# Performance work log

Measured on AMD Instinct MI355X. Metric: run time of the kernel, lower is better.

## Reference

```python
import jax, jax.numpy as jnp
import numpy as np

B, T, D, U = 2, 512, 768, 768


def setup_inputs() -> dict:
    key = jax.random.key(0)
    kx, kv, ku, kw = jax.random.split(key, 4)
    x = jax.random.normal(kx, (B, T, D), dtype=jnp.float32)
    # glorot-ish scaled params
    V_a = jax.random.normal(kv, (U,), dtype=jnp.float32) * (1.0 / np.sqrt(U))
    U_a = jax.random.normal(ku, (D, U), dtype=jnp.float32) * (1.0 / np.sqrt(D))
    b_u = jnp.zeros((U,), dtype=jnp.float32)
    W_a = jax.random.normal(kw, (D, U), dtype=jnp.float32) * (1.0 / np.sqrt(D))
    return {"x": x, "V_a": V_a, "U_a": U_a, "b_u": b_u, "W_a": W_a}


def reference(x, V_a, U_a, b_u, W_a):
    # Bahdanau additive self-attention, fully batched (replaces the per-timestep loop).
    # wx[b,i,u] = x[b,i] @ W_a  (query projection; original recomputed this per step)
    wx = jnp.einsum('bid,du->biu', x, W_a)
    # ux[b,j,u] = x[b,j] @ U_a + b_u  (the _uxpb term)
    ux = jnp.einsum('bjd,du->bju', x, U_a) + b_u
    # e[b,i,j] = V_a . tanh(wx[b,i] + ux[b,j])
    e = jnp.einsum('biju,u->bij', jnp.tanh(wx[:, :, None, :] + ux[:, None, :, :]), V_a)
    # original: exp / sum over keys == softmax over axis j (no mask path)
    at = jax.nn.softmax(e, axis=2)
    # context[b,i,d] = sum_j at[b,i,j] * x[b,j,d]
    return jnp.einsum('bij,bjd->bid', at, x)
```

## Files before the change

kernel.cpp:

```cpp
#include <hip/hip_runtime.h>
#include <hip/hip_bf16.h>

#define BB 2
#define TT 512
#define DD 768
#define UU 768
#define NR (BB*TT)
#define CC 2.8853900817779268f
#define HC 1.4426950408889634f

typedef __attribute__((ext_vector_type(8))) short short8v;
typedef __attribute__((ext_vector_type(4))) float float4v;
typedef __attribute__((ext_vector_type(4))) unsigned short ushort4v;
typedef _Float16 half4v __attribute__((ext_vector_type(4)));

static __device__ __forceinline__ float fexp2(float x) { return __builtin_amdgcn_exp2f(x); }
static __device__ __forceinline__ float frcp(float x)  { return __builtin_amdgcn_rcpf(x); }
static __device__ __forceinline__ unsigned short bf16rn(float f) {
    unsigned u = __builtin_bit_cast(unsigned, f);
    u += 0x7FFFu + ((u >> 16) & 1u);
    return (unsigned short)(u >> 16);
}
static __device__ __forceinline__ float bf16tof(unsigned short h) {
    return __builtin_bit_cast(float, ((unsigned)h) << 16);
}

__global__ __launch_bounds__(256) void prep_split(
    const float* __restrict__ x,
    const float* __restrict__ Wm,
    const float* __restrict__ Um,
    unsigned short* __restrict__ xhi, unsigned short* __restrict__ xlo,
    unsigned short* __restrict__ WThi, unsigned short* __restrict__ WTlo,
    unsigned short* __restrict__ UThi, unsigned short* __restrict__ UTlo)
{
    const int mode = blockIdx.z;
    const int t = threadIdx.x;

    if (mode == 2) {
        const int blk = blockIdx.y * 12 + blockIdx.x;
        const float4* src = (const float4*)x + (size_t)blk * 1024;
        #pragma unroll
        for (int i = 0; i < 4; ++i) {
            const int idx = i * 256 + t;
            const float4 v = src[idx];
            ushort4v h, l;
            h.x = bf16rn(v.x); l.x = bf16rn(v.x - bf16tof(h.x));
            h.y = bf16rn(v.y); l.y = bf16rn(v.y - bf16tof(h.y));
            h.z = bf16rn(v.z); l.z = bf16rn(v.z - bf16tof(h.z));
            h.w = bf16rn(v.w); l.w = bf16rn(v.w - bf16tof(h.w));
            const size_t off = (size_t)blk * 4096 + (size_t)idx * 4;
            *(ushort4v*)(xhi + off) = h;
            *(ushort4v*)(xlo + off) = l;
        }
        return;
    }
    if (blockIdx.y >= 12) return;

    const float* __restrict__ S = (mode == 0) ? Wm : Um;
    unsigned short* __restrict__ Thi = (mode == 0) ? WThi : UThi;
    unsigned short* __restrict__ Tlo = (mode == 0) ? WTlo : UTlo;

    __shared__ float tile[64][65];
    const int d0 = blockIdx.y * 64;
    const int u0 = blockIdx.x * 64;

    #pragma unroll
    for (int i = 0; i < 4; ++i) {
        const int f4 = i * 256 + t;
        const int r  = f4 >> 4;
        const int c4 = f4 & 15;
        const float4 v = *(const float4*)(S + (size_t)(d0 + r) * UU + u0 + c4 * 4);
        tile[r][c4 * 4 + 0] = v.x;
        tile[r][c4 * 4 + 1] = v.y;
        tile[r][c4 * 4 + 2] = v.z;
        tile[r][c4 * 4 + 3] = v.w;
    }
    __syncthreads();
    #pragma unroll
    for (int i = 0; i < 2; ++i) {
        const int cid = i * 256 + t;
        const int ur  = cid >> 3;
        const int kc  = cid & 7;
        short8v H, L;
        #pragma unroll
        for (int j = 0; j < 8; ++j) {
            const float f = tile[kc * 8 + j][ur];
            const unsigned short h = bf16rn(f);
            H[j] = (short)h;
            L[j] = (short)bf16rn(f - bf16tof(h));
        }
        const size_t off = (size_t)(u0 + ur) * DD + d0 + kc * 8;
        *(short8v*)(Thi + off) = H;
        *(short8v*)(Tlo + off) = L;
    }
}

__global__ __launch_bounds__(256) void gemm_mfma(
    const unsigned short* __restrict__ xhi, const unsigned short* __restrict__ xlo,
    const unsigned short* __restrict__ WThi, const unsigned short* __restrict__ WTlo,
    const unsigned short* __restrict__ UThi, const unsigned short* __restrict__ UTlo,
    const float* __restrict__ bu,
    float* __restrict__ EW4,
    _Float16* __restrict__ EUTH)
{
    const int mode = blockIdx.z;
    const unsigned short* __restrict__ Ahi = mode ? UThi : WThi;
    const unsigned short* __restrict__ Alo = mode ? UTlo : WTlo;

    __shared__ unsigned short lds[4 * 4096];

    const int tid  = threadIdx.x;
    const int lane = tid & 63;
    const int wid  = tid >> 6;
    const int wm   = wid >> 1, wn = wid & 1;
    const int u0   = blockIdx.y * 64;
    const int r0t  = blockIdx.x * 64;

    const int srow0 = tid >> 3;
    const int srow1 = srow0 + 32;
    const int sc0   = tid & 7;
    const int sw0   = (sc0 ^ (srow0 & 7)) << 3;

    short8v g0, g1, g2, g3, g4, g5, g6, g7;

#define LOADSTEP(K0) { \
    const size_t ka = (size_t)(K0) + sc0 * 8; \
    g0 = *(const short8v*)(Ahi + (size_t)(u0 + srow0) * DD + ka); \
    g1 = *(const short8v*)(Ahi + (size_t)(u0 + srow1) * DD + ka); \
    g2 = *(const short8v*)(Alo + (size_t)(u0 + srow0) * DD + ka); \
    g3 = *(const short8v*)(Alo + (size_t)(u0 + srow1) * DD + ka); \
    g4 = *(const short8v*)(xhi + (size_t)(r0t + srow0) * DD + ka); \
    g5 = *(const short8v*)(xhi + (size_t)(r0t + srow1) * DD + ka); \
    g6 = *(const short8v*)(xlo + (size_t)(r0t + srow0) * DD + ka); \
    g7 = *(const short8v*)(xlo + (size_t)(r0t + srow1) * DD + ka); }

#define WRITESTEP { \
    *(short8v*)&lds[0 * 4096 + srow0 * 64 + sw0] = g0; \
    *(short8v*)&lds[0 * 4096 + srow1 * 64 + sw0] = g1; \
    *(short8v*)&lds[1 * 4096 + srow0 * 64 + sw0] = g2; \
    *(short8v*)&lds[1 * 4096 + srow1 * 64 + sw0] = g3; \
    *(short8v*)&lds[2 * 4096 + srow0 * 64 + sw0] = g4; \
    *(short8v*)&lds[2 * 4096 + srow1 * 64 + sw0] = g5; \
    *(short8v*)&lds[3 * 4096 + srow0 * 64 + sw0] = g6; \
    *(short8v*)&lds[3 * 4096 + srow1 * 64 + sw0] = g7; }

    float4v acc[2][2] = {};

    LOADSTEP(0);
    for (int s = 0; s < 12; ++s) {
        __syncthreads();
        WRITESTEP;
        __syncthreads();
        if (s < 11) LOADSTEP((s + 1) * 64);

        short8v ah[2][2], al[2][2], bh[2][2], bl[2][2];
        #pragma unroll
        for (int f = 0; f < 2; ++f) {
            const int arow = wm * 32 + f * 16 + (lane & 15);
            const int brow = wn * 32 + f * 16 + (lane & 15);
            #pragma unroll
            for (int kk = 0; kk < 2; ++kk) {
                const int ck = kk * 4 + (lane >> 4);
                ah[f][kk] = *(const short8v*)&lds[0 * 4096 + arow * 64 + (((ck ^ (arow & 7))) << 3)];
                al[f][kk] = *(const short8v*)&lds[1 * 4096 + arow * 64 + (((ck ^ (arow & 7))) << 3)];
                bh[f][kk] = *(const short8v*)&lds[2 * 4096 + brow * 64 + (((ck ^ (brow & 7))) << 3)];
                bl[f][kk] = *(const short8v*)&lds[3 * 4096 + brow * 64 + (((ck ^ (brow & 7))) << 3)];
            }
        }
        #pragma unroll
        for (int kk = 0; kk < 2; ++kk)
            #pragma unroll
            for (int m = 0; m < 2; ++m)
                #pragma unroll
                for (int n = 0; n < 2; ++n) {
                    acc[m][n] = __builtin_amdgcn_mfma_f32_16x16x32_bf16(ah[m][kk], bh[n][kk], acc[m][n], 0, 0, 0);
                    acc[m][n] = __builtin_amdgcn_mfma_f32_16x16x32_bf16(ah[m][kk], bl[n][kk], acc[m][n], 0, 0, 0);
                    acc[m][n] = __builtin_amdgcn_mfma_f32_16x16x32_bf16(al[m][kk], bh[n][kk], acc[m][n], 0, 0, 0);
                }
    }

    #pragma unroll
    for (int m = 0; m < 2; ++m) {
        #pragma unroll
        for (int n = 0; n < 2; ++n) {
            const int ub = u0 + wm * 32 + m * 16 + ((lane >> 4) << 2);
            const int r  = r0t + wn * 32 + n * 16 + (lane & 15);
            if (mode == 0) {
                float* dst = EW4 + ((size_t)(r >> 2) * UU + ub) * 4 + (r & 3);
                #pragma unroll
                for (int reg = 0; reg < 4; ++reg)
                    dst[reg * 4] = fexp2(acc[m][n][reg] * CC);
            } else {
                const int b = r >> 9, j = r & 511;
                const float4 bv = *(const float4*)(bu + ub);
                half4v o;
                o[0] = (_Float16)fexp2((acc[m][n][0] + bv.x) * HC);
                o[1] = (_Float16)fexp2((acc[m][n][1] + bv.y) * HC);
                o[2] = (_Float16)fexp2((acc[m][n][2] + bv.z) * HC);
                o[3] = (_Float16)fexp2((acc[m][n][3] + bv.w) * HC);
                *(half4v*)(EUTH + ((size_t)(b * 192 + (ub >> 2)) * 512 + j) * 4) = o;
            }
        }
    }
#undef LOADSTEP
#undef WRITESTEP
}

__global__ __launch_bounds__(1024) void attn_fused(
    const float* __restrict__ x,
    const float* __restrict__ V_a,
    const float* __restrict__ EW4,
    const _Float16* __restrict__ EUTH,
    float* __restrict__ out)
{
    extern __shared__ float smem[];
    float4* sw4  = (float4*)smem;
    float*  vv   = smem + 3072;
    float*  xchg = smem + 4096;
    float*  red  = smem + 6144;
    float4* at4  = (float4*)(smem + 8192);
    float*  part = smem;
    float*  iv   = smem + 12352;

    const int tid  = threadIdx.x;
    const int lane = tid & 63;
    const int j    = tid & 511;
    const int uh   = tid >> 9;

    const int bid = blockIdx.x;
    const int blk = (bid & 7) * 32 + (bid >> 3);

    const int r0 = blk * 4;
    const int b  = r0 >> 9;

    if (tid < UU) {
        sw4[tid] = ((const float4*)EW4)[(size_t)blk * UU + tid];
        vv[tid]  = V_a[tid];
    }
    __syncthreads();

    const half4v* __restrict__ eqh =
        (const half4v*)EUTH + (size_t)(b * 192 + uh * 96) * 512 + j;

    float acc0 = 0.f, acc1 = 0.f, acc2 = 0.f, acc3 = 0.f;

#define PAIR(E0, E1, u0) { \
    const float4 S0 = sw4[(u0)]; \
    const float4 S1 = sw4[(u0) + 1]; \
    const float v0 = vv[(u0)], v1 = vv[(u0) + 1]; \
    { const float da = fmaf((E0), S0.x, 1.f), db = fmaf((E1), S1.x, 1.f); \
      float n = v0 * db; n = fmaf(v1, da, n); \
      acc0 = fmaf(n, frcp(da * db), acc0); } \
    { const float da = fmaf((E0), S0.y, 1.f), db = fmaf((E1), S1.y, 1.f); \
      float n = v0 * db; n = fmaf(v1, da, n); \
      acc1 = fmaf(n, frcp(da * db), acc1); } \
    { const float da = fmaf((E0), S0.z, 1.f), db = fmaf((E1), S1.z, 1.f); \
      float n = v0 * db; n = fmaf(v1, da, n); \
      acc2 = fmaf(n, frcp(da * db), acc2); } \
    { const float da = fmaf((E0), S0.w, 1.f), db = fmaf((E1), S1.w, 1.f); \
      float n = v0 * db; n = fmaf(v1, da, n); \
      acc3 = fmaf(n, frcp(da * db), acc3); } }
#define QUADH(H, UB) { \
    const float e0 = (float)(H)[0], e1 = (float)(H)[1]; \
    const float e2 = (float)(H)[2], e3 = (float)(H)[3]; \
    PAIR(e0 * e0, e1 * e1, (UB)); PAIR(e2 * e2, e3 * e3, (UB) + 2); }

    const int ubase = uh * 384 / 4;
    const int ub0 = uh * 384;

    half4v c0 = eqh[0 * 512], c1 = eqh[1 * 512], c2 = eqh[2 * 512], c3 = eqh[3 * 512];
    #pragma unroll 1
    for (int c = 0; c < 23; ++c) {
        const int q = 4 * c;
        half4v n0 = eqh[(size_t)(q + 4) * 512];
        half4v n1 = eqh[(size_t)(q + 5) * 512];
        half4v n2 = eqh[(size_t)(q + 6) * 512];
        half4v n3 = eqh[(size_t)(q + 7) * 512];
        const int ub = ub0 + 16 * c;
        QUADH(c0, ub); QUADH(c1, ub + 4); QUADH(c2, ub + 8); QUADH(c3, ub + 12);
        c0 = n0; c1 = n1; c2 = n2; c3 = n3;
    }
    QUADH(c0, ub0 + 368); QUADH(c1, ub0 + 372); QUADH(c2, ub0 + 376); QUADH(c3, ub0 + 380);
    (void)ubase;

    if (uh) *(float4*)&xchg[j * 4] = make_float4(acc0, acc1, acc2, acc3);
    __syncthreads();
    if (!uh) {
        const float4 o = *(float4*)&xchg[j * 4];
        acc0 += o.x; acc1 += o.y; acc2 += o.z; acc3 += o.w;
    }

    float m0 = acc0, m1 = acc1, m2 = acc2, m3 = acc3;
    #pragma unroll
    for (int off = 32; off; off >>= 1) {
        m0 = fminf(m0, __shfl_xor(m0, off, 64));
        m1 = fminf(m1, __shfl_xor(m1, off, 64));
        m2 = fminf(m2, __shfl_xor(m2, off, 64));
        m3 = fminf(m3, __shfl_xor(m3, off, 64));
    }
    if (tid < 512 && lane == 0) {
        const int w = tid >> 6;
        red[0 * 8 + w] = m0; red[1 * 8 + w] = m1;
        red[2 * 8 + w] = m2; red[3 * 8 + w] = m3;
    }
    __syncthreads();
    float M0 = red[0], M1 = red[8], M2 = red[16], M3 = red[24];
    #pragma unroll
    for (int k = 1; k < 8; ++k) {
        M0 = fminf(M0, red[0 * 8 + k]);
        M1 = fminf(M1, red[1 * 8 + k]);
        M2 = fminf(M2, red[2 * 8 + k]);
        M3 = fminf(M3, red[3 * 8 + k]);
    }

    const float p0 = fexp2(CC * (M0 - acc0));
    const float p1 = fexp2(CC * (M1 - acc1));
    const float p2 = fexp2(CC * (M2 - acc2));
    const float p3 = fexp2(CC * (M3 - acc3));
    float s0 = p0, s1 = p1, s2 = p2, s3 = p3;
    #pragma unroll
    for (int off = 32; off; off >>= 1) {
        s0 += __shfl_xor(s0, off, 64);
        s1 += __shfl_xor(s1, off, 64);
        s2 += __shfl_xor(s2, off, 64);
        s3 += __shfl_xor(s3, off, 64);
    }
    __syncthreads();
    if (tid < 512 && lane == 0) {
        const int w = tid >> 6;
        red[32 + 0 * 8 + w] = s0; red[32 + 1 * 8 + w] = s1;
        red[32 + 2 * 8 + w] = s2; red[32 + 3 * 8 + w] = s3;
    }
    __syncthreads();
    if (tid == 0) {
        float S0 = red[32], S1 = red[40], S2 = red[48], S3 = red[56];
        #pragma unroll
        for (int k = 1; k < 8; ++k) {
            S0 += red[32 + k]; S1 += red[40 + k];
            S2 += red[48 + k]; S3 += red[56 + k];
        }
        iv[0] = frcp(S0); iv[1] = frcp(S1); iv[2] = frcp(S2); iv[3] = frcp(S3);
    }
    if (tid < 512) at4[j] = make_float4(p0, p1, p2, p3);
    __syncthreads();

    const int w16 = tid >> 6;
    const int jw  = w16 * 32;
    const float* __restrict__ xb = x + (size_t)b * TT * DD + (size_t)jw * DD + 4 * lane;
    float4 z4 = {0.f, 0.f, 0.f, 0.f};
    float4 pc00 = z4, pc01 = z4, pc02 = z4;
    float4 pc10 = z4, pc11 = z4, pc12 = z4;
    float4 pc20 = z4, pc21 = z4, pc22 = z4;
    float4 pc30 = z4, pc31 = z4, pc32 = z4;

#define F4(dst, a, xv) { dst.x = fmaf(a, xv.x, dst.x); dst.y = fmaf(a, xv.y, dst.y); \
                         dst.z = fmaf(a, xv.z, dst.z); dst.w = fmaf(a, xv.w, dst.w); }
    #pragma unroll 2
    for (int jj = 0; jj < 32; ++jj) {
        const float4 a = at4[jw + jj];
        const float* xr = xb + (size_t)jj * DD;
        const float4 x0 = *(const float4*)(xr);
        const float4 x1 = *(const float4*)(xr + 256);
        const float4 x2 = *(const float4*)(xr + 512);
        F4(pc00, a.x, x0); F4(pc01, a.x, x1); F4(pc02, a.x, x2);
        F4(pc10, a.y, x0); F4(pc11, a.y, x1); F4(pc12, a.y, x2);
        F4(pc20, a.z, x0); F4(pc21, a.z, x1); F4(pc22, a.z, x2);
        F4(pc30, a.w, x0); F4(pc31, a.w, x1); F4(pc32, a.w, x2);
    }
    __syncthreads();

#define REDPASS(PA, PB, PCc, R) { \
    *(float4*)&part[w16 * 772 + 4 * lane]       = PA; \
    *(float4*)&part[w16 * 772 + 256 + 4 * lane] = PB; \
    *(float4*)&part[w16 * 772 + 512 + 4 * lane] = PCc; \
    __syncthreads(); \
    if (tid < 768) { \
        float ssum = 0.f; \
        _Pragma("unroll") \
        for (int w2 = 0; w2 < 16; ++w2) ssum += part[w2 * 772 + tid]; \
        out[(size_t)(r0 + (R)) * DD + tid] = ssum * iv[(R)]; \
    } \
    __syncthreads(); }

    REDPASS(pc00, pc01, pc02, 0);
    REDPASS(pc10, pc11, pc12, 1);
    REDPASS(pc20, pc21, pc22, 2);
    REDPASS(pc30, pc31, pc32, 3);
}

extern "C" void kernel_launch(void* const* d_in, const int* in_sizes, int n_in,
                              void* d_out, int out_size, void* d_ws, size_t ws_size,
                              hipStream_t stream)
{
    const float* x   = (const float*)d_in[0];
    const float* V_a = (const float*)d_in[1];
    const float* U_a = (const float*)d_in[2];
    const float* b_u = (const float*)d_in[3];
    const float* W_a = (const float*)d_in[4];
    float* out = (float*)d_out;

    float* EW4 = (float*)d_ws;
    _Float16* EUTH = (_Float16*)(EW4 + (size_t)UU * NR);
    unsigned short* xhi  = (unsigned short*)(EUTH + (size_t)BB * UU * TT);
    unsigned short* xlo  = xhi + (size_t)NR * DD;
    unsigned short* WThi = xlo + (size_t)NR * DD;
    unsigned short* WTlo = WThi + (size_t)UU * DD;
    unsigned short* UThi = WTlo + (size_t)UU * DD;
    unsigned short* UTlo = UThi + (size_t)UU * DD;

    hipLaunchKernelGGL(prep_split, dim3(12, 16, 3), dim3(256), 0, stream,
                       x, W_a, U_a, xhi, xlo, WThi, WTlo, UThi, UTlo);

    hipLaunchKernelGGL(gemm_mfma, dim3(16, 12, 2), dim3(256), 0, stream,
                       xhi, xlo, WThi, WTlo, UThi, UTlo, b_u, EW4, EUTH);

    const int ldsB = 12356 * sizeof(float);
    hipLaunchKernelGGL(attn_fused, dim3(NR / 4), dim3(1024), ldsB, stream,
                       x, V_a, EW4, EUTH, out);
}
```

Baseline: 84.75 us.

## Store key exp terms in fp32 and combine four tanh terms per reciprocal

The key-side exponentials are now written in fp32 with the full 2*log2e scale, instead of fp16 half-scale values that had to be squared on load. The attention inner loop merges four tanh terms into one reciprocal rather than two, which cuts the number of rcp instructions. Query exponentials and V_a are read straight from global memory (uniform per block, so cached) rather than staged in LDS, which drops the preload and its barrier. The cost is twice the bytes for the key array and a larger product of four denominators, which raises the risk of overflow or precision loss.

```diff
diff --git a/kernel.cpp b/kernel.cpp
--- a/kernel.cpp
+++ b/kernel.cpp
@@ -7,12 +7,10 @@
 #define UU 768
 #define NR (BB*TT)
 #define CC 2.8853900817779268f
-#define HC 1.4426950408889634f
 
 typedef __attribute__((ext_vector_type(8))) short short8v;
 typedef __attribute__((ext_vector_type(4))) float float4v;
 typedef __attribute__((ext_vector_type(4))) unsigned short ushort4v;
-typedef _Float16 half4v __attribute__((ext_vector_type(4)));
 
 static __device__ __forceinline__ float fexp2(float x) { return __builtin_amdgcn_exp2f(x); }
 static __device__ __forceinline__ float frcp(float x)  { return __builtin_amdgcn_rcpf(x); }
@@ -101,7 +99,7 @@
     const unsigned short* __restrict__ UThi, const unsigned short* __restrict__ UTlo,
     const float* __restrict__ bu,
     float* __restrict__ EW4,
-    _Float16* __restrict__ EUTH)
+    float* __restrict__ EUT)
 {
     const int mode = blockIdx.z;
     const unsigned short* __restrict__ Ahi = mode ? UThi : WThi;
@@ -193,12 +191,12 @@
             } else {
                 const int b = r >> 9, j = r & 511;
                 const float4 bv = *(const float4*)(bu + ub);
-                half4v o;
-                o[0] = (_Float16)fexp2((acc[m][n][0] + bv.x) * HC);
-                o[1] = (_Float16)fexp2((acc[m][n][1] + bv.y) * HC);
-                o[2] = (_Float16)fexp2((acc[m][n][2] + bv.z) * HC);
-                o[3] = (_Float16)fexp2((acc[m][n][3] + bv.w) * HC);
-                *(half4v*)(EUTH + ((size_t)(b * 192 + (ub >> 2)) * 512 + j) * 4) = o;
+                float4v o;
+                o[0] = fexp2((acc[m][n][0] + bv.x) * CC);
+                o[1] = fexp2((acc[m][n][1] + bv.y) * CC);
+                o[2] = fexp2((acc[m][n][2] + bv.z) * CC);
+                o[3] = fexp2((acc[m][n][3] + bv.w) * CC);
+                *(float4v*)(EUT + (size_t)b * (UU * TT) + (size_t)(ub >> 2) * (TT * 4) + j * 4) = o;
             }
         }
     }
@@ -210,15 +208,13 @@
     const float* __restrict__ x,
     const float* __restrict__ V_a,
     const float* __restrict__ EW4,
-    const _Float16* __restrict__ EUTH,
+    const float* __restrict__ EUT,
     float* __restrict__ out)
 {
     extern __shared__ float smem[];
-    float4* sw4  = (float4*)smem;
-    float*  vv   = smem + 3072;
-    float*  xchg = smem + 4096;
-    float*  red  = smem + 6144;
-    float4* at4  = (float4*)(smem + 8192);
+    float*  red  = smem;
+    float*  xchg = smem + 64;
+    float4* at4  = (float4*)(smem + 2112);
     float*  part = smem;
     float*  iv   = smem + 12352;
 
@@ -233,55 +229,48 @@
     const int r0 = blk * 4;
     const int b  = r0 >> 9;
 
-    if (tid < UU) {
-        sw4[tid] = ((const float4*)EW4)[(size_t)blk * UU + tid];
-        vv[tid]  = V_a[tid];
-    }
-    __syncthreads();
-
-    const half4v* __restrict__ eqh =
-        (const half4v*)EUTH + (size_t)(b * 192 + uh * 96) * 512 + j;
+    const float4* __restrict__ ew4q = (const float4*)EW4 + (size_t)blk * UU + uh * 384;
+    const float4* __restrict__ vp4  = (const float4*)V_a + uh * 96;
+    const float4* __restrict__ eq   =
+        (const float4*)(EUT + (size_t)b * UU * TT) + (size_t)uh * 96 * 512 + j;
 
     float acc0 = 0.f, acc1 = 0.f, acc2 = 0.f, acc3 = 0.f;
 
-#define PAIR(E0, E1, u0) { \
-    const float4 S0 = sw4[(u0)]; \
-    const float4 S1 = sw4[(u0) + 1]; \
-    const float v0 = vv[(u0)], v1 = vv[(u0) + 1]; \
-    { const float da = fmaf((E0), S0.x, 1.f), db = fmaf((E1), S1.x, 1.f); \
-      float n = v0 * db; n = fmaf(v1, da, n); \
-      acc0 = fmaf(n, frcp(da * db), acc0); } \
-    { const float da = fmaf((E0), S0.y, 1.f), db = fmaf((E1), S1.y, 1.f); \
-      float n = v0 * db; n = fmaf(v1, da, n); \
-      acc1 = fmaf(n, frcp(da * db), acc1); } \
-    { const float da = fmaf((E0), S0.z, 1.f), db = fmaf((E1), S1.z, 1.f); \
-      float n = v0 * db; n = fmaf(v1, da, n); \
-      acc2 = fmaf(n, frcp(da * db), acc2); } \
-    { const float da = fmaf((E0), S0.w, 1.f), db = fmaf((E1), S1.w, 1.f); \
-      float n = v0 * db; n = fmaf(v1, da, n); \
-      acc3 = fmaf(n, frcp(da * db), acc3); } }
-#define QUADH(H, UB) { \
-    const float e0 = (float)(H)[0], e1 = (float)(H)[1]; \
-    const float e2 = (float)(H)[2], e3 = (float)(H)[3]; \
-    PAIR(e0 * e0, e1 * e1, (UB)); PAIR(e2 * e2, e3 * e3, (UB) + 2); }
-
-    const int ubase = uh * 384 / 4;
-    const int ub0 = uh * 384;
-
-    half4v c0 = eqh[0 * 512], c1 = eqh[1 * 512], c2 = eqh[2 * 512], c3 = eqh[3 * 512];
+#define ROW4(E4, S0, S1, S2, S3, V4, F, ACC) { \
+    const float d0 = fmaf((E4).x, S0.F, 1.f); \
+    const float d1 = fmaf((E4).y, S1.F, 1.f); \
+    const float d2 = fmaf((E4).z, S2.F, 1.f); \
+    const float d3 = fmaf((E4).w, S3.F, 1.f); \
+    float n01 = (V4).x * d1; n01 = fmaf((V4).y, d0, n01); \
+    float n23 = (V4).z * d3; n23 = fmaf((V4).w, d2, n23); \
+    const float dd01 = d0 * d1, dd23 = d2 * d3; \
+    float n = n01 * dd23; n = fmaf(n23, dd01, n); \
+    ACC = fmaf(n, frcp(dd01 * dd23), ACC); }
+#define QUAD4(E4, q) { \
+    const float4 S0 = ew4q[4 * (q)]; \
+    const float4 S1 = ew4q[4 * (q) + 1]; \
+    const float4 S2 = ew4q[4 * (q) + 2]; \
+    const float4 S3 = ew4q[4 * (q) + 3]; \
+    const float4 V4 = vp4[(q)]; \
+    ROW4(E4, S0, S1, S2, S3, V4, x, acc0); \
+    ROW4(E4, S0, S1, S2, S3, V4, y, acc1); \
+    ROW4(E4, S0, S1, S2, S3, V4, z, acc2); \
+    ROW4(E4, S0, S1, S2, S3, V4, w, acc3); }
+
+    float4 c0 = eq[0 * 512], c1 = eq[1 * 512], c2 = eq[2 * 512], c3 = eq[3 * 512];
     #pragma unroll 1
     for (int c = 0; c < 23; ++c) {
         const int q = 4 * c;
-        half4v n0 = eqh[(size_t)(q + 4) * 512];
-        half4v n1 = eqh[(size_t)(q + 5) * 512];
-        half4v n2 = eqh[(size_t)(q + 6) * 512];
-        half4v n3 = eqh[(size_t)(q + 7) * 512];
-        const int ub = ub0 + 16 * c;
-        QUADH(c0, ub); QUADH(c1, ub + 4); QUADH(c2, ub + 8); QUADH(c3, ub + 12);
-        c0 = n0; c1 = n1; c2 = n2; c3 = n3;
-    }
-    QUADH(c0, ub0 + 368); QUADH(c1, ub0 + 372); QUADH(c2, ub0 + 376); QUADH(c3, ub0 + 380);
-    (void)ubase;
+        float4 n0_ = eq[(size_t)(q + 4) * 512];
+        float4 n1_ = eq[(size_t)(q + 5) * 512];
+        float4 n2_ = eq[(size_t)(q + 6) * 512];
+        float4 n3_ = eq[(size_t)(q + 7) * 512];
+        QUAD4(c0, q); QUAD4(c1, q + 1); QUAD4(c2, q + 2); QUAD4(c3, q + 3);
+        c0 = n0_; c1 = n1_; c2 = n2_; c3 = n3_;
+    }
+    QUAD4(c0, 92); QUAD4(c1, 93); QUAD4(c2, 94); QUAD4(c3, 95);
+#undef QUAD4
+#undef ROW4
 
     if (uh) *(float4*)&xchg[j * 4] = make_float4(acc0, acc1, acc2, acc3);
     __syncthreads();
@@ -367,6 +356,7 @@
         F4(pc20, a.z, x0); F4(pc21, a.z, x1); F4(pc22, a.z, x2);
         F4(pc30, a.w, x0); F4(pc31, a.w, x1); F4(pc32, a.w, x2);
     }
+#undef F4
     __syncthreads();
 
 #define REDPASS(PA, PB, PCc, R) { \
@@ -386,6 +376,7 @@
     REDPASS(pc10, pc11, pc12, 1);
     REDPASS(pc20, pc21, pc22, 2);
     REDPASS(pc30, pc31, pc32, 3);
+#undef REDPASS
 }
 
 extern "C" void kernel_launch(void* const* d_in, const int* in_sizes, int n_in,
@@ -400,8 +391,8 @@
     float* out = (float*)d_out;
 
     float* EW4 = (float*)d_ws;
-    _Float16* EUTH = (_Float16*)(EW4 + (size_t)UU * NR);
-    unsigned short* xhi  = (unsigned short*)(EUTH + (size_t)BB * UU * TT);
+    float* EUT = EW4 + (size_t)UU * NR;
+    unsigned short* xhi  = (unsigned short*)(EUT + (size_t)BB * UU * TT);
     unsigned short* xlo  = xhi + (size_t)NR * DD;
     unsigned short* WThi = xlo + (size_t)NR * DD;
     unsigned short* WTlo = WThi + (size_t)UU * DD;
@@ -412,9 +403,9 @@
                        x, W_a, U_a, xhi, xlo, WThi, WTlo, UThi, UTlo);
 
     hipLaunchKernelGGL(gemm_mfma, dim3(16, 12, 2), dim3(256), 0, stream,
-                       xhi, xlo, WThi, WTlo, UThi, UTlo, b_u, EW4, EUTH);
+                       xhi, xlo, WThi, WTlo, UThi, UTlo, b_u, EW4, EUT);
 
     const int ldsB = 12356 * sizeof(float);
     hipLaunchKernelGGL(attn_fused, dim3(NR / 4), dim3(1024), ldsB, stream,
-                       x, V_a, EW4, EUTH, out);
-}
+                       x, V_a, EW4, EUT, out);
+}
```

Result: slower. 111.4 us (+31.4%).
